# Kernel optimization log

Hardware: AMD Instinct MI355X
Metric: run time of the kernel (lower is better)

The kernel has to match this reference:

```python
import jax, jax.numpy as jnp
import numpy as np

HIDDEN = 2048
NUM_HEADS = 8
NUM_KV_HEADS = 1
HEAD_DIM = 256
ROPE_THETA = 10000.0
T = 2048  # num tokens (single causal prefill sequence)
Q_SIZE = NUM_HEADS * HEAD_DIM        # 2048
KV_SIZE = NUM_KV_HEADS * HEAD_DIM    # 256


def _apply_rope(x, positions):
    # x: [T, n_heads, head_dim], neox style (rotate halves)
    half = HEAD_DIM // 2
    inv_freq = 1.0 / (ROPE_THETA ** (jnp.arange(half, dtype=jnp.float32) * 2.0 / HEAD_DIM))
    ang = positions.astype(jnp.float32)[:, None] * inv_freq[None, :]   # [T, half]
    cos = jnp.cos(ang)[:, None, :]
    sin = jnp.sin(ang)[:, None, :]
    x1, x2 = jnp.split(x, 2, axis=-1)
    return jnp.concatenate([x1 * cos - x2 * sin, x2 * cos + x1 * sin], axis=-1)


def setup_inputs() -> dict:
    key = jax.random.key(0)
    k1, k2, k3 = jax.random.split(key, 3)
    hidden_states = jax.random.normal(k1, (T, HIDDEN), dtype=jnp.float32)
    Wqkv = jax.random.normal(k2, (Q_SIZE + 2 * KV_SIZE, HIDDEN), dtype=jnp.float32) * 0.02
    Wo = jax.random.normal(k3, (HIDDEN, Q_SIZE), dtype=jnp.float32) * 0.02
    positions = jnp.arange(T, dtype=jnp.int32)
    return {"positions": positions, "hidden_states": hidden_states, "Wqkv": Wqkv, "Wo": Wo}


def reference(positions, hidden_states, Wqkv, Wo):
    scaling = HEAD_DIM ** -0.5
    qkv = hidden_states @ Wqkv.T                                   # [T, Q+2KV]
    q = qkv[:, :Q_SIZE].reshape(T, NUM_HEADS, HEAD_DIM)
    k = qkv[:, Q_SIZE:Q_SIZE + KV_SIZE].reshape(T, NUM_KV_HEADS, HEAD_DIM)
    v = qkv[:, Q_SIZE + KV_SIZE:].reshape(T, NUM_KV_HEADS, HEAD_DIM)
    q = _apply_rope(q, positions)
    k = _apply_rope(k, positions)
    # GQA: group query heads over kv heads
    g = NUM_HEADS // NUM_KV_HEADS
    qg = q.reshape(T, NUM_KV_HEADS, g, HEAD_DIM)
    scores = jnp.einsum('qhgd,khd->hgqk', qg, k) * scaling         # [kv, g, T, T]
    causal = jnp.arange(T)[:, None] >= jnp.arange(T)[None, :]
    scores = jnp.where(causal[None, None], scores, jnp.finfo(scores.dtype).min)
    probs = jax.nn.softmax(scores, axis=-1)
    attn = jnp.einsum('hgqk,khd->qhgd', probs, v).reshape(T, Q_SIZE)
    return attn @ Wo.T
```

## Files before the change

### kernel.cpp

```cpp
#include <hip/hip_runtime.h>
#include <hip/hip_bf16.h>

typedef __bf16 bf16x8 __attribute__((ext_vector_type(8)));
typedef __bf16 bf16x4 __attribute__((ext_vector_type(4)));
typedef float floatx4 __attribute__((ext_vector_type(4)));

__device__ __forceinline__ float fast_exp2(float x) {
    return __builtin_amdgcn_exp2f(x);
}

__device__ __forceinline__ void lds_barrier() {
    asm volatile("s_waitcnt lgkmcnt(0)\n\ts_barrier" ::: "memory");
}

template<int CTRL>
__device__ __forceinline__ float fdpp(float x) {
    union { float f; int i; } u, v;
    u.f = x;
    v.i = __builtin_amdgcn_update_dpp(0, u.i, CTRL, 0xf, 0xf, true);
    return v.f;
}
__device__ __forceinline__ float row16_max(float x) {
    x = fmaxf(x, fdpp<0xB1>(x));
    x = fmaxf(x, fdpp<0x4E>(x));
    x = fmaxf(x, fdpp<0x128>(x));
    x = fmaxf(x, fdpp<0x124>(x));
    return x;
}
__device__ __forceinline__ float row16_sum(float x) {
    x += fdpp<0xB1>(x);
    x += fdpp<0x4E>(x);
    x += fdpp<0x128>(x);
    x += fdpp<0x124>(x);
    return x;
}

__global__ __launch_bounds__(256) void cast_all(const float* __restrict__ hid,
                                                const float* __restrict__ wqkv,
                                                const float* __restrict__ wo,
                                                __bf16* __restrict__ Ah,
                                                __bf16* __restrict__ Wqkvh,
                                                __bf16* __restrict__ Woh) {
    const int n1 = 1048576, n2 = 1310720;
    int i = blockIdx.x * 256 + threadIdx.x;
    const float* in;
    __bf16* out;
    int j;
    if (i < n1) { in = hid; out = Ah; j = i; }
    else if (i < n1 + n2) { in = wqkv; out = Wqkvh; j = i - n1; }
    else { in = wo; out = Woh; j = i - n1 - n2; }
    float4 v = ((const float4*)in)[j];
    bf16x4 o;
    o[0] = (__bf16)v.x; o[1] = (__bf16)v.y; o[2] = (__bf16)v.z; o[3] = (__bf16)v.w;
    ((bf16x4*)out)[j] = o;
}

template<typename OutT>
__global__ __launch_bounds__(256) void gemm_bt(const __bf16* __restrict__ A,
                                               const __bf16* __restrict__ B,
                                               OutT* __restrict__ C,
                                               int M, int N, int K) {
    __shared__ __attribute__((aligned(16))) __bf16 As[128 * 64];
    __shared__ __attribute__((aligned(16))) __bf16 Bs[128 * 64];

    int tid = threadIdx.x, lane = tid & 63, w = tid >> 6;
    int wm = (w >> 1) * 64, wn = (w & 1) * 64;
    int bm0 = blockIdx.x * 128, bn0 = blockIdx.y * 128;
    int r = lane & 15, q4 = lane >> 4;
    int rr = lane >> 2, qq = lane & 3;

    const __bf16* Agp[4];
    const __bf16* Bgp[4];
    __bf16* Asd[4];
    __bf16* Bsd[4];
#pragma unroll
    for (int j = 0; j < 4; j++) {
        int c = w * 4 + j;
        int kk = c >> 3, g = c & 7;
        Agp[j] = A + (size_t)(bm0 + g * 16 + rr) * K + kk * 32 + qq * 8;
        Bgp[j] = B + (size_t)(bn0 + g * 16 + rr) * K + kk * 32 + qq * 8;
        Asd[j] = &As[c * 512 + lane * 8];
        Bsd[j] = &Bs[c * 512 + lane * 8];
    }

    floatx4 acc[4][4];
#pragma unroll
    for (int i = 0; i < 4; i++)
#pragma unroll
        for (int j = 0; j < 4; j++) acc[i][j] = (floatx4)0.f;

    bf16x8 ar[4], br[4];
#pragma unroll
    for (int j = 0; j < 4; j++) {
        ar[j] = *(const bf16x8*)Agp[j];
        br[j] = *(const bf16x8*)Bgp[j];
    }

    for (int k0 = 0; k0 < K; k0 += 64) {
        lds_barrier();
#pragma unroll
        for (int j = 0; j < 4; j++) {
            *(bf16x8*)Asd[j] = ar[j];
            *(bf16x8*)Bsd[j] = br[j];
        }
        if (k0 + 64 < K) {
#pragma unroll
            for (int j = 0; j < 4; j++) {
                ar[j] = *(const bf16x8*)(Agp[j] + k0 + 64);
                br[j] = *(const bf16x8*)(Bgp[j] + k0 + 64);
            }
        }
        lds_barrier();

#pragma unroll
        for (int kk = 0; kk < 2; kk++) {
            bf16x8 a[4], b[4];
#pragma unroll
            for (int mt = 0; mt < 4; mt++)
                a[mt] = *(const bf16x8*)&As[(kk * 8 + (wm >> 4) + mt) * 512 + r * 32 + q4 * 8];
#pragma unroll
            for (int nt = 0; nt < 4; nt++)
                b[nt] = *(const bf16x8*)&Bs[(kk * 8 + (wn >> 4) + nt) * 512 + r * 32 + q4 * 8];
#pragma unroll
            for (int mt = 0; mt < 4; mt++)
#pragma unroll
                for (int nt = 0; nt < 4; nt++)
                    acc[mt][nt] = __builtin_amdgcn_mfma_f32_16x16x32_bf16(a[mt], b[nt], acc[mt][nt], 0, 0, 0);
        }
    }

#pragma unroll
    for (int mt = 0; mt < 4; mt++)
#pragma unroll
        for (int nt = 0; nt < 4; nt++) {
            int row = bm0 + wm + mt * 16 + q4 * 4;
            int col = bn0 + wn + nt * 16 + r;
#pragma unroll
            for (int i = 0; i < 4; i++)
                C[(size_t)(row + i) * N + col] = (OutT)acc[mt][nt][i];
        }
}

__global__ __launch_bounds__(256) void rope_vtrans(const __bf16* __restrict__ qkv,
                                                   const int* __restrict__ positions,
                                                   __bf16* __restrict__ Qo,
                                                   __bf16* __restrict__ Ko,
                                                   __bf16* __restrict__ Vt) {
    __shared__ float tile[32][33];
    int b = blockIdx.x;
    if (b < 9216) {
        int idx = b * 256 + threadIdx.x;
        int i = idx & 127;
        int th = idx >> 7;
        int head = th % 9;
        int t = th / 9;
        float invf = expf(-(float)i * 0.07195578415606394f);
        float ang = (float)positions[t] * invf;
        float s = sinf(ang), c = cosf(ang);
        size_t off = (size_t)t * 2560 + (head < 8 ? head * 256 : 2048);
        float x1 = (float)qkv[off + i];
        float x2 = (float)qkv[off + i + 128];
        if (head < 8) {
            const float qs = 0.09016844f;
            __bf16* dst = Qo + (size_t)t * 2048 + head * 256;
            dst[i]       = (__bf16)((x1 * c - x2 * s) * qs);
            dst[i + 128] = (__bf16)((x2 * c + x1 * s) * qs);
        } else {
            __bf16* dst = Ko + (size_t)t * 256;
            dst[i]       = (__bf16)(x1 * c - x2 * s);
            dst[i + 128] = (__bf16)(x2 * c + x1 * s);
        }
    } else {
        int bb = b - 9216;
        int bt = bb & 63;
        int bc = bb >> 6;
        int tx = threadIdx.x & 31;
        int ty0 = threadIdx.x >> 5;
#pragma unroll
        for (int ty = ty0; ty < 32; ty += 8)
            tile[ty][tx] = (float)qkv[(size_t)(bt * 32 + ty) * 2560 + 2304 + bc * 32 + tx];
        __syncthreads();
#pragma unroll
        for (int ty = ty0; ty < 32; ty += 8)
            Vt[(size_t)(bc * 32 + ty) * 2048 + bt * 32 + tx] = (__bf16)tile[tx][ty];
    }
}

__global__ __launch_bounds__(256) void attn_kernel(const __bf16* __restrict__ Q,
                                                   const __bf16* __restrict__ Kg,
                                                   const __bf16* __restrict__ Vt,
                                                   __bf16* __restrict__ Opart,
                                                   float2* __restrict__ Ml) {
    __shared__ __attribute__((aligned(16))) __bf16 Ks[32 * 264];
    __shared__ __attribute__((aligned(16))) __bf16 Vs[256 * 40];
    __shared__ __attribute__((aligned(16))) __bf16 Ps[4][16][40];

    int hg = blockIdx.x;
    int rs = 407 - (int)blockIdx.y;
    int k, base;
    if (rs < 24)       { k = 1; base = 0; }
    else if (rs < 72)  { k = 2; base = 24; }
    else if (rs < 144) { k = 3; base = 72; }
    else if (rs < 240) { k = 4; base = 144; }
    else if (rs < 360) { k = 5; base = 240; }
    else               { k = 6; base = 360; }
    int idx = rs - base;
    int s = idx % k;
    int g = (k - 1) * 24 + idx / k;
    int slot = base + idx - s;

    int start = s * 384;
    int end = g * 16 + 16;
    if (end > start + 384) end = start + 384;
    int ntiles = (end - start + 31) >> 5;

    int tid = threadIdx.x, lane = tid & 63, w = tid >> 6;
    int r = lane & 15, q4 = lane >> 4;
    int h = hg * 4 + w;

    int krow = w * 8 + (lane & 7);
    int kcol = (lane >> 3) * 32;
    int vrow = w * 64 + lane;
    __bf16* kd = &Ks[krow * 264 + kcol];
    __bf16* vd = &Vs[vrow * 40];

    bf16x8 qf[8];
    {
        const __bf16* qrow = Q + (size_t)(g * 16 + r) * 2048 + h * 256 + q4 * 8;
#pragma unroll
        for (int ks = 0; ks < 8; ks++) qf[ks] = *(const bf16x8*)(qrow + ks * 32);
    }

    floatx4 acc[16];
#pragma unroll
    for (int i = 0; i < 16; i++) acc[i] = (floatx4)0.f;
    float m_i[4] = {-3e38f, -3e38f, -3e38f, -3e38f};
    float l_i[4] = {0.f, 0.f, 0.f, 0.f};

    bf16x8 kr[4], vr[4];
    {
        const __bf16* kp = Kg + (size_t)(start + krow) * 256 + kcol;
        const __bf16* vp = Vt + (size_t)vrow * 2048 + start;
#pragma unroll
        for (int j = 0; j < 4; j++) {
            kr[j] = *(const bf16x8*)(kp + j * 8);
            vr[j] = *(const bf16x8*)(vp + j * 8);
        }
    }

    for (int t = 0; t < ntiles; t++) {
        int kt0 = start + t * 32;
        lds_barrier();
#pragma unroll
        for (int j = 0; j < 4; j++) {
            *(bf16x8*)(kd + j * 8) = kr[j];
            *(bf16x8*)(vd + j * 8) = vr[j];
        }
        if (t + 1 < ntiles) {
            const __bf16* kp = Kg + (size_t)(kt0 + 32 + krow) * 256 + kcol;
            const __bf16* vp = Vt + (size_t)vrow * 2048 + kt0 + 32;
#pragma unroll
            for (int j = 0; j < 4; j++) {
                kr[j] = *(const bf16x8*)(kp + j * 8);
                vr[j] = *(const bf16x8*)(vp + j * 8);
            }
        }
        lds_barrier();

        floatx4 sc[2];
        sc[0] = (floatx4)0.f; sc[1] = (floatx4)0.f;
#pragma unroll
        for (int ks = 0; ks < 8; ks++) {
#pragma unroll
            for (int nt = 0; nt < 2; nt++) {
                bf16x8 kf = *(const bf16x8*)&Ks[(nt * 16 + r) * 264 + ks * 32 + q4 * 8];
                sc[nt] = __builtin_amdgcn_mfma_f32_16x16x32_bf16(qf[ks], kf, sc[nt], 0, 0, 0);
            }
        }
        if (kt0 + 31 > g * 16) {
            int qbase = g * 16 + q4 * 4;
#pragma unroll
            for (int nt = 0; nt < 2; nt++) {
                int kpos = kt0 + nt * 16 + r;
#pragma unroll
                for (int i = 0; i < 4; i++)
                    if (kpos > qbase + i) sc[nt][i] = -3e38f;
            }
        }
        float alpha[4];
#pragma unroll
        for (int i = 0; i < 4; i++) {
            float m = row16_max(fmaxf(sc[0][i], sc[1][i]));
            float mn = fmaxf(m_i[i], m);
            alpha[i] = fast_exp2(m_i[i] - mn);
            m_i[i] = mn;
        }
        floatx4 p[2];
#pragma unroll
        for (int i = 0; i < 4; i++) {
            p[0][i] = fast_exp2(sc[0][i] - m_i[i]);
            p[1][i] = fast_exp2(sc[1][i] - m_i[i]);
            float sum = row16_sum(p[0][i] + p[1][i]);
            l_i[i] = l_i[i] * alpha[i] + sum;
        }
#pragma unroll
        for (int n16 = 0; n16 < 16; n16++)
#pragma unroll
            for (int i = 0; i < 4; i++) acc[n16][i] *= alpha[i];

#pragma unroll
        for (int nt = 0; nt < 2; nt++)
#pragma unroll
            for (int i = 0; i < 4; i++)
                Ps[w][q4 * 4 + i][(nt * 16 + r) ^ (q4 << 3)] = (__bf16)p[nt][i];
        __builtin_amdgcn_wave_barrier();
        bf16x8 pf = *(const bf16x8*)&Ps[w][r][(q4 * 8) ^ ((r >> 2) << 3)];
        __builtin_amdgcn_wave_barrier();

#pragma unroll
        for (int n16 = 0; n16 < 16; n16++) {
            bf16x8 vf = *(const bf16x8*)&Vs[(n16 * 16 + r) * 40 + q4 * 8];
            acc[n16] = __builtin_amdgcn_mfma_f32_16x16x32_bf16(pf, vf, acc[n16], 0, 0, 0);
        }
    }

    size_t base_row = (size_t)(slot + s) * 128 + hg * 64 + w * 16;
#pragma unroll
    for (int n16 = 0; n16 < 16; n16++)
#pragma unroll
        for (int i = 0; i < 4; i++)
            Opart[(base_row + q4 * 4 + i) * 256 + n16 * 16 + r] = (__bf16)acc[n16][i];
    if (r == 0) {
#pragma unroll
        for (int i = 0; i < 4; i++)
            Ml[base_row + q4 * 4 + i] = make_float2(m_i[i], l_i[i]);
    }
}

__global__ __launch_bounds__(256) void combine_kernel(const __bf16* __restrict__ Opart,
                                                      const float2* __restrict__ Ml,
                                                      __bf16* __restrict__ attnb) {
    int wid = blockIdx.x * 4 + (threadIdx.x >> 6);
    int lane = threadIdx.x & 63;
    int t = wid >> 3, h = wid & 7;
    int g = t >> 4, row = t & 15;
    int hg = h >> 2, w = h & 3;
    int nsp = g / 24 + 1;
    int full = g / 24, rem = g % 24;
    int fg = 12 * full * (full + 1) + rem * (full + 1);

    float ms[6], ls[6];
    size_t rbase[6];
    float M = -3e38f;
    for (int s = 0; s < nsp; s++) {
        rbase[s] = (size_t)(fg + s) * 128 + hg * 64 + w * 16 + row;
        float2 ml = Ml[rbase[s]];
        ms[s] = ml.x; ls[s] = ml.y;
        M = fmaxf(M, ml.x);
    }
    float L = 0.f;
    float o[4] = {0.f, 0.f, 0.f, 0.f};
    for (int s = 0; s < nsp; s++) {
        float wsc = fast_exp2(ms[s] - M);
        L += ls[s] * wsc;
        bf16x4 v = *(const bf16x4*)&Opart[rbase[s] * 256 + lane * 4];
#pragma unroll
        for (int j = 0; j < 4; j++) o[j] += wsc * (float)v[j];
    }
    float inv = 1.f / L;
    bf16x4 ov;
#pragma unroll
    for (int j = 0; j < 4; j++) ov[j] = (__bf16)(o[j] * inv);
    *(bf16x4*)&attnb[(size_t)t * 2048 + h * 256 + lane * 4] = ov;
}

extern "C" void kernel_launch(void* const* d_in, const int* in_sizes, int n_in,
                              void* d_out, int out_size, void* d_ws, size_t ws_size,
                              hipStream_t stream) {
    const int* positions = (const int*)d_in[0];
    const float* hidden  = (const float*)d_in[1];
    const float* Wqkv    = (const float*)d_in[2];
    const float* Wo      = (const float*)d_in[3];
    float* out = (float*)d_out;

    char* ws = (char*)d_ws;
    const size_t MB = 1024 * 1024;
    __bf16* Ah    = (__bf16*)(ws + 0 * MB);
    __bf16* Woh   = (__bf16*)(ws + 8 * MB);
    __bf16* Qb    = (__bf16*)(ws + 16 * MB);
    __bf16* Kb    = (__bf16*)(ws + 24 * MB);
    __bf16* Vtb   = (__bf16*)(ws + 25 * MB);
    __bf16* Wqkvh = (__bf16*)(ws + 26 * MB);
    __bf16* qkvb  = (__bf16*)(ws + 36 * MB);
    __bf16* Opart = (__bf16*)(ws + 26 * MB);
    float2* Ml    = (float2*)(ws + 52 * MB);
    __bf16* attnb = Ah;

    cast_all<<<13312, 256, 0, stream>>>(hidden, Wqkv, Wo, Ah, Wqkvh, Woh);

    gemm_bt<__bf16><<<dim3(16, 20), 256, 0, stream>>>(Ah, Wqkvh, qkvb, 2048, 2560, 2048);

    rope_vtrans<<<9728, 256, 0, stream>>>(qkvb, positions, Qb, Kb, Vtb);

    attn_kernel<<<dim3(2, 408), 256, 0, stream>>>(Qb, Kb, Vtb, Opart, Ml);
    combine_kernel<<<4096, 256, 0, stream>>>(Opart, Ml, attnb);

    gemm_bt<float><<<dim3(16, 16), 256, 0, stream>>>(attnb, Woh, out, 2048, 2048, 2048);
}
```

Measured before the change: 248.7 us.

## Rework LDS layouts in GEMM and attention staging, add attention occupancy hint

The GEMM moves from a pre-swizzled fragment-block LDS layout to a row-major layout padded to 72 elements, with each thread loading one row segment of 32 contiguous elements. The attention kernel goes the other way: K and V tiles are stored in LDS in MFMA fragment order, so every lane reads one contiguous 16-byte chunk at lane*8 and no padding is needed. It also adds a launch_bounds minimum of 4 blocks. The aims are cheaper LDS reads in attention and simpler, more coalesced global loads in the GEMM, at the cost of possible bank conflicts in the padded GEMM layout and register pressure from the occupancy hint.

```diff
diff --git a/kernel.cpp b/kernel.cpp
--- a/kernel.cpp
+++ b/kernel.cpp
@@ -60,54 +60,46 @@
                                                const __bf16* __restrict__ B,
                                                OutT* __restrict__ C,
                                                int M, int N, int K) {
-    __shared__ __attribute__((aligned(16))) __bf16 As[128 * 64];
-    __shared__ __attribute__((aligned(16))) __bf16 Bs[128 * 64];
+    __shared__ __attribute__((aligned(16))) __bf16 As[128 * 72];
+    __shared__ __attribute__((aligned(16))) __bf16 Bs[128 * 72];
 
     int tid = threadIdx.x, lane = tid & 63, w = tid >> 6;
     int wm = (w >> 1) * 64, wn = (w & 1) * 64;
     int bm0 = blockIdx.x * 128, bn0 = blockIdx.y * 128;
     int r = lane & 15, q4 = lane >> 4;
-    int rr = lane >> 2, qq = lane & 3;
-
-    const __bf16* Agp[4];
-    const __bf16* Bgp[4];
-    __bf16* Asd[4];
-    __bf16* Bsd[4];
+
+    int srow = tid & 127;
+    int scol = (tid >> 7) * 32;
+    const __bf16* Ag = A + (size_t)(bm0 + srow) * K + scol;
+    const __bf16* Bg = B + (size_t)(bn0 + srow) * K + scol;
+    __bf16* Asd = &As[srow * 72 + scol];
+    __bf16* Bsd = &Bs[srow * 72 + scol];
+
+    floatx4 acc[4][4];
+#pragma unroll
+    for (int i = 0; i < 4; i++)
+#pragma unroll
+        for (int j = 0; j < 4; j++) acc[i][j] = (floatx4)0.f;
+
+    bf16x8 ar[4], br[4];
 #pragma unroll
     for (int j = 0; j < 4; j++) {
-        int c = w * 4 + j;
-        int kk = c >> 3, g = c & 7;
-        Agp[j] = A + (size_t)(bm0 + g * 16 + rr) * K + kk * 32 + qq * 8;
-        Bgp[j] = B + (size_t)(bn0 + g * 16 + rr) * K + kk * 32 + qq * 8;
-        Asd[j] = &As[c * 512 + lane * 8];
-        Bsd[j] = &Bs[c * 512 + lane * 8];
-    }
-
-    floatx4 acc[4][4];
-#pragma unroll
-    for (int i = 0; i < 4; i++)
-#pragma unroll
-        for (int j = 0; j < 4; j++) acc[i][j] = (floatx4)0.f;
-
-    bf16x8 ar[4], br[4];
-#pragma unroll
-    for (int j = 0; j < 4; j++) {
-        ar[j] = *(const bf16x8*)Agp[j];
-        br[j] = *(const bf16x8*)Bgp[j];
+        ar[j] = *(const bf16x8*)(Ag + j * 8);
+        br[j] = *(const bf16x8*)(Bg + j * 8);
     }
 
     for (int k0 = 0; k0 < K; k0 += 64) {
         lds_barrier();
 #pragma unroll
         for (int j = 0; j < 4; j++) {
-            *(bf16x8*)Asd[j] = ar[j];
-            *(bf16x8*)Bsd[j] = br[j];
+            *(bf16x8*)(Asd + j * 8) = ar[j];
+            *(bf16x8*)(Bsd + j * 8) = br[j];
         }
         if (k0 + 64 < K) {
 #pragma unroll
             for (int j = 0; j < 4; j++) {
-                ar[j] = *(const bf16x8*)(Agp[j] + k0 + 64);
-                br[j] = *(const bf16x8*)(Bgp[j] + k0 + 64);
+                ar[j] = *(const bf16x8*)(Ag + k0 + 64 + j * 8);
+                br[j] = *(const bf16x8*)(Bg + k0 + 64 + j * 8);
             }
         }
         lds_barrier();
@@ -117,10 +109,10 @@
             bf16x8 a[4], b[4];
 #pragma unroll
             for (int mt = 0; mt < 4; mt++)
-                a[mt] = *(const bf16x8*)&As[(kk * 8 + (wm >> 4) + mt) * 512 + r * 32 + q4 * 8];
+                a[mt] = *(const bf16x8*)&As[(wm + mt * 16 + r) * 72 + kk * 32 + q4 * 8];
 #pragma unroll
             for (int nt = 0; nt < 4; nt++)
-                b[nt] = *(const bf16x8*)&Bs[(kk * 8 + (wn >> 4) + nt) * 512 + r * 32 + q4 * 8];
+                b[nt] = *(const bf16x8*)&Bs[(wn + nt * 16 + r) * 72 + kk * 32 + q4 * 8];
 #pragma unroll
             for (int mt = 0; mt < 4; mt++)
 #pragma unroll
@@ -186,13 +178,13 @@
     }
 }
 
-__global__ __launch_bounds__(256) void attn_kernel(const __bf16* __restrict__ Q,
-                                                   const __bf16* __restrict__ Kg,
-                                                   const __bf16* __restrict__ Vt,
-                                                   __bf16* __restrict__ Opart,
-                                                   float2* __restrict__ Ml) {
-    __shared__ __attribute__((aligned(16))) __bf16 Ks[32 * 264];
-    __shared__ __attribute__((aligned(16))) __bf16 Vs[256 * 40];
+__global__ __launch_bounds__(256, 4) void attn_kernel(const __bf16* __restrict__ Q,
+                                                      const __bf16* __restrict__ Kg,
+                                                      const __bf16* __restrict__ Vt,
+                                                      __bf16* __restrict__ Opart,
+                                                      float2* __restrict__ Ml) {
+    __shared__ __attribute__((aligned(16))) __bf16 Ks[16 * 512];
+    __shared__ __attribute__((aligned(16))) __bf16 Vs[16 * 512];
     __shared__ __attribute__((aligned(16))) __bf16 Ps[4][16][40];
 
     int hg = blockIdx.x;
@@ -220,9 +212,9 @@
 
     int krow = w * 8 + (lane & 7);
     int kcol = (lane >> 3) * 32;
-    int vrow = w * 64 + lane;
-    __bf16* kd = &Ks[krow * 264 + kcol];
-    __bf16* vd = &Vs[vrow * 40];
+    __bf16* kd = &Ks[((lane >> 3) * 2 + (w >> 1)) * 512 + ((w & 1) * 8 + (lane & 7)) * 8];
+    __bf16* vd = &Vs[w * 2048 + lane * 8];
+    const __bf16* vgbase = Vt + (size_t)(w * 64 + (lane & 15)) * 2048 + (lane >> 4) * 8;
 
     bf16x8 qf[8];
     {
@@ -240,11 +232,10 @@
     bf16x8 kr[4], vr[4];
     {
         const __bf16* kp = Kg + (size_t)(start + krow) * 256 + kcol;
-        const __bf16* vp = Vt + (size_t)vrow * 2048 + start;
 #pragma unroll
         for (int j = 0; j < 4; j++) {
             kr[j] = *(const bf16x8*)(kp + j * 8);
-            vr[j] = *(const bf16x8*)(vp + j * 8);
+            vr[j] = *(const bf16x8*)(vgbase + (size_t)j * 16 * 2048 + start);
         }
     }
 
@@ -253,16 +244,15 @@
         lds_barrier();
 #pragma unroll
         for (int j = 0; j < 4; j++) {
-            *(bf16x8*)(kd + j * 8) = kr[j];
-            *(bf16x8*)(vd + j * 8) = vr[j];
+            *(bf16x8*)(kd + j * 128) = kr[j];
+            *(bf16x8*)(vd + j * 512) = vr[j];
         }
         if (t + 1 < ntiles) {
             const __bf16* kp = Kg + (size_t)(kt0 + 32 + krow) * 256 + kcol;
-            const __bf16* vp = Vt + (size_t)vrow * 2048 + kt0 + 32;
 #pragma unroll
             for (int j = 0; j < 4; j++) {
                 kr[j] = *(const bf16x8*)(kp + j * 8);
-                vr[j] = *(const bf16x8*)(vp + j * 8);
+                vr[j] = *(const bf16x8*)(vgbase + (size_t)j * 16 * 2048 + kt0 + 32);
             }
         }
         lds_barrier();
@@ -273,7 +263,7 @@
         for (int ks = 0; ks < 8; ks++) {
 #pragma unroll
             for (int nt = 0; nt < 2; nt++) {
-                bf16x8 kf = *(const bf16x8*)&Ks[(nt * 16 + r) * 264 + ks * 32 + q4 * 8];
+                bf16x8 kf = *(const bf16x8*)&Ks[(ks * 2 + nt) * 512 + lane * 8];
                 sc[nt] = __builtin_amdgcn_mfma_f32_16x16x32_bf16(qf[ks], kf, sc[nt], 0, 0, 0);
             }
         }
@@ -319,7 +309,7 @@
 
 #pragma unroll
         for (int n16 = 0; n16 < 16; n16++) {
-            bf16x8 vf = *(const bf16x8*)&Vs[(n16 * 16 + r) * 40 + q4 * 8];
+            bf16x8 vf = *(const bf16x8*)&Vs[n16 * 512 + lane * 8];
             acc[n16] = __builtin_amdgcn_mfma_f32_16x16x32_bf16(pf, vf, acc[n16], 0, 0, 0);
         }
     }
```

Result: slower. 365.3 us (+46.9%).
